# Kernel optimization log

Hardware: AMD Instinct MI355X
Metric: run time of the kernel (lower is better)

The kernel has to match this reference:

```python
import jax, jax.numpy as jnp
import numpy as np

DIM = 1024
T, B = 1024, 32


def setup_inputs() -> dict:
    key = jax.random.key(0)
    ks = jax.random.split(key, 6)
    x = jax.random.normal(ks[0], (T, B, DIM), dtype=jnp.float32)
    h0 = jnp.zeros((B, DIM), dtype=jnp.float32)
    W_zr = 0.02 * jax.random.normal(ks[1], (2 * DIM, DIM), dtype=jnp.float32)
    U_zr = 0.02 * jax.random.normal(ks[2], (2 * DIM, DIM), dtype=jnp.float32)
    W_h = 0.02 * jax.random.normal(ks[3], (DIM, DIM), dtype=jnp.float32)
    U_h = 0.02 * jax.random.normal(ks[4], (DIM, DIM), dtype=jnp.float32)
    b_zr = jnp.zeros((2 * DIM,), dtype=jnp.float32)
    b_h = jnp.zeros((DIM,), dtype=jnp.float32)
    return {"x": x, "h0": h0, "W_zr": W_zr, "U_zr": U_zr,
            "W_h": W_h, "U_h": U_h, "b_zr": b_zr, "b_h": b_h}


def _gru(x, h0, W_zr, U_zr, W_h, U_h, b_zr, b_h):
    dim = h0.shape[-1]
    # Precompute input projections for all timesteps (batched GEMM).
    xzr = jnp.einsum('tbd,ed->tbe', x, W_zr) + b_zr   # [T,B,2D]
    xh = jnp.einsum('tbd,ed->tbe', x, W_h) + b_h      # [T,B,D]
    U_z, U_r = U_zr[:dim], U_zr[dim:]

    def step(h_prev, inputs):
        xzr_t, xh_t = inputs
        z = jax.nn.sigmoid(xzr_t[:, :dim] + h_prev @ U_z.T)
        r = jax.nn.sigmoid(xzr_t[:, dim:] + h_prev @ U_r.T)
        h_tilde = jnp.tanh(xh_t + (r * h_prev) @ U_h.T)
        h = (1.0 - z) * h_prev + z * h_tilde
        return h, h

    _, hs = jax.lax.scan(step, h0, (xzr, xh))
    return hs  # [T,B,D]


def reference(x, h0, W_zr, U_zr, W_h, U_h, b_zr, b_h):
    return _gru(x, h0, W_zr, U_zr, W_h, U_h, b_zr, b_h)
```

## Files before the change

kernel.cpp:

```cpp
#include <hip/hip_runtime.h>


typedef __attribute__((ext_vector_type(8))) __bf16 bf16x8;
typedef __attribute__((ext_vector_type(4))) float f32x4;
typedef unsigned short ushort_t;
typedef unsigned long long u64;

#define DIM_ 1024
#define BATCH_ 32
#define T_ 1024
#define NC_ 3072

static constexpr size_t OFF_P     = 0;
static constexpr size_t OFF_XBF   = 201326592;
static constexpr size_t OFF_WBF   = OFF_XBF + 67108864;
static constexpr size_t OFF_UZR   = OFF_WBF + 6291456;
static constexpr size_t OFF_UH    = OFF_UZR + 4194304;
static constexpr size_t OFF_HB    = OFF_UH  + 2097152;
static constexpr size_t OFF_RH    = OFF_HB  + 65536;
static constexpr size_t OFF_FLAGS = OFF_RH  + 65536;

__device__ __forceinline__ float b2f(ushort_t u) {
  union { float f; unsigned i; } v;
  v.i = ((unsigned)u) << 16;
  return v.f;
}
__device__ __forceinline__ ushort_t f2b(float f) {
  union { float f; unsigned i; } v;
  v.f = f;
  unsigned r = v.i + 0x7fffu + ((v.i >> 16) & 1u);
  return (ushort_t)(r >> 16);
}

__device__ __forceinline__ void st_u32_sc(void* p, unsigned v) {
  asm volatile("global_store_dword %0, %1, off sc0 sc1" ::"v"(p), "v"(v)
               : "memory");
}
__device__ __forceinline__ unsigned ld_u32_sc(const void* p) {
  unsigned r;
  asm volatile("global_load_dword %0, %1, off sc0 sc1\n\ts_waitcnt vmcnt(0)"
               : "=v"(r) : "v"(p) : "memory");
  return r;
}
__device__ __forceinline__ u64 ld_u64_sc(const void* p) {
  u64 r;
  asm volatile("global_load_dwordx2 %0, %1, off sc0 sc1" : "=v"(r) : "v"(p));
  return r;
}
__device__ __forceinline__ void vm_drain() {
  asm volatile("s_waitcnt vmcnt(0)" ::: "memory");
}

__global__ void cvt_f32_bf16x4(const float4* __restrict__ src,
                               uint2* __restrict__ dst, int n4) {
  int i = blockIdx.x * blockDim.x + threadIdx.x;
  int st = gridDim.x * blockDim.x;
  for (; i < n4; i += st) {
    float4 v = src[i];
    unsigned a = (unsigned)f2b(v.x) | ((unsigned)f2b(v.y) << 16);
    unsigned b = (unsigned)f2b(v.z) | ((unsigned)f2b(v.w) << 16);
    dst[i] = make_uint2(a, b);
  }
}

__global__ void zero_flags(unsigned* f) { f[threadIdx.x] = 0u; }

__global__ __launch_bounds__(256) void gemm_xw(
    const ushort_t* __restrict__ A, const ushort_t* __restrict__ Bm,
    const float* __restrict__ bzr, const float* __restrict__ bh,
    ushort_t* __restrict__ C) {
  __shared__ ushort_t As[128][40];
  __shared__ ushort_t Bs[128][40];
  const int bi = blockIdx.x;
  const int p = bi / 192;
  const int q = bi % 192;
  const int i0 = (p * 8 + (q & 7)) * 128;
  const int n0 = (q >> 3) * 128;
  const int tid = threadIdx.x;
  const int w = tid >> 6, l = tid & 63;
  const int wr = w >> 1, wc = w & 1;
  const int quad = l >> 4, lr = l & 15;

  f32x4 acc[4][4] = {};
  for (int kc = 0; kc < 1024; kc += 32) {
    __syncthreads();
#pragma unroll
    for (int j = 0; j < 2; ++j) {
      int c = j * 256 + tid;
      int r = c >> 2, pp = c & 3;
      *(int4*)(&As[r][pp * 8]) =
          *(const int4*)(A + (size_t)(i0 + r) * 1024 + kc + pp * 8);
      *(int4*)(&Bs[r][pp * 8]) =
          *(const int4*)(Bm + (size_t)(n0 + r) * 1024 + kc + pp * 8);
    }
    __syncthreads();
    bf16x8 af[4], bfr[4];
#pragma unroll
    for (int mb = 0; mb < 4; ++mb)
      af[mb] = *(const bf16x8*)(&As[wr * 64 + mb * 16 + lr][quad * 8]);
#pragma unroll
    for (int nb = 0; nb < 4; ++nb)
      bfr[nb] = *(const bf16x8*)(&Bs[wc * 64 + nb * 16 + lr][quad * 8]);
#pragma unroll
    for (int mb = 0; mb < 4; ++mb)
#pragma unroll
      for (int nb = 0; nb < 4; ++nb)
        acc[mb][nb] = __builtin_amdgcn_mfma_f32_16x16x32_bf16(
            af[mb], bfr[nb], acc[mb][nb], 0, 0, 0);
  }
#pragma unroll
  for (int nb = 0; nb < 4; ++nb) {
    int col = n0 + wc * 64 + nb * 16 + lr;
    float bias = (col < 2048) ? bzr[col] : bh[col - 2048];
#pragma unroll
    for (int mb = 0; mb < 4; ++mb) {
#pragma unroll
      for (int reg = 0; reg < 4; ++reg) {
        int row = i0 + wr * 64 + mb * 16 + quad * 4 + reg;
        C[(size_t)row * NC_ + col] = f2b(acc[mb][nb][reg] + bias);
      }
    }
  }
}

__device__ __forceinline__ void group_barrier(unsigned* gflags, int gg,
                                              unsigned gen, int tid) {
  vm_drain();
  __syncthreads();
  if (tid == 0) st_u32_sc(gflags + gg, gen);
  if (tid < 32) {
    while (ld_u32_sc(gflags + tid) < gen) __builtin_amdgcn_s_sleep(1);
  }
  __syncthreads();
}

__global__ __launch_bounds__(256, 1) void gru_scan(
    const ushort_t* __restrict__ P, const ushort_t* __restrict__ Uzr,
    const ushort_t* __restrict__ Uh, const float* __restrict__ h0,
    ushort_t* __restrict__ Hb, ushort_t* __restrict__ RH,
    unsigned* __restrict__ flags, float* __restrict__ out) {
  const int g = blockIdx.x;
  const int G = g >> 5, gg = g & 31;
  const int rb0 = G * 16;
  const int cs = gg * 32;
  const int tid = threadIdx.x;
  const int w = tid >> 6, l = tid & 63;
  const int quad = l >> 4, lr = l & 15;
  unsigned* gflags = flags + G * 32;

  __shared__ ushort_t StageL[16][1032];
  __shared__ float Hl[16][33];
  __shared__ f32x4 red[2][64];

  const int ctA = w >> 1, cbA = w & 1;
  const int khB = w >> 1, cbB = w & 1;
  const int eA = cs + cbA * 16 + lr;
  const int eB = cs + cbB * 16 + lr;

  bf16x8 wa[32];
  {
    const ushort_t* urow = Uzr + (size_t)(ctA * 1024 + eA) * DIM_;
#pragma unroll
    for (int it = 0; it < 32; ++it)
      wa[it] = *(const bf16x8*)(urow + it * 32 + quad * 8);
  }
  bf16x8 wb[16];
  {
    const ushort_t* urow = Uh + (size_t)eB * DIM_ + khB * 512;
#pragma unroll
    for (int it = 0; it < 16; ++it)
      wb[it] = *(const bf16x8*)(urow + it * 32 + quad * 8);
  }

  {
    int rr = tid >> 4, cp = tid & 15;
    int c0 = cp * 2;
    float v0 = h0[(rb0 + rr) * DIM_ + cs + c0];
    float v1 = h0[(rb0 + rr) * DIM_ + cs + c0 + 1];
    Hl[rr][c0] = v0;
    Hl[rr][c0 + 1] = v1;
    unsigned pk = (unsigned)f2b(v0) | ((unsigned)f2b(v1) << 16);
    st_u32_sc(&Hb[(size_t)(rb0 + rr) * DIM_ + cs + c0], pk);
  }

  float pA[4], pB[4];
  {
    const size_t prow = (size_t)rb0 * NC_;
#pragma unroll
    for (int reg = 0; reg < 4; ++reg) {
      int br = quad * 4 + reg;
      pA[reg] = b2f(P[prow + (size_t)br * NC_ + ctA * 1024 + eA]);
      pB[reg] = b2f(P[prow + (size_t)br * NC_ + 2048 + eB]);
    }
  }

  unsigned gen = 1;
  group_barrier(gflags, gg, gen, tid);

  for (int t = 0; t < T_; ++t) {
    {
      u64 tmp[16];
#pragma unroll
      for (int j = 0; j < 16; ++j)
        tmp[j] =
            ld_u64_sc((const u64*)(Hb + (size_t)(rb0 + j) * DIM_) + tid);
      vm_drain();
#pragma unroll
      for (int j = 0; j < 16; ++j) *(u64*)&StageL[j][tid * 4] = tmp[j];
    }
    __syncthreads();

    f32x4 acc = {0.f, 0.f, 0.f, 0.f};
#pragma unroll
    for (int it = 0; it < 32; ++it) {
      bf16x8 a = *(const bf16x8*)&StageL[lr][it * 32 + quad * 8];
      acc = __builtin_amdgcn_mfma_f32_16x16x32_bf16(a, wa[it], acc, 0, 0, 0);
    }
    float zv[4];
#pragma unroll
    for (int reg = 0; reg < 4; ++reg) {
      int br = quad * 4 + reg;
      float pre = acc[reg] + pA[reg];
      float sv = 1.f / (1.f + __expf(-pre));
      if (ctA == 0) {
        zv[reg] = sv;
      } else {
        float hv = Hl[br][cbA * 16 + lr];
        unsigned own = f2b(sv * hv);
        unsigned oth = (unsigned)__shfl_xor((int)own, 1);
        if ((l & 1) == 0) {
          unsigned pk = own | (oth << 16);
          st_u32_sc(&RH[(size_t)(rb0 + br) * DIM_ + eA], pk);
        }
      }
    }
    ++gen;
    group_barrier(gflags, gg, gen, tid);

    {
      u64 tmp[16];
#pragma unroll
      for (int j = 0; j < 16; ++j)
        tmp[j] =
            ld_u64_sc((const u64*)(RH + (size_t)(rb0 + j) * DIM_) + tid);
      vm_drain();
#pragma unroll
      for (int j = 0; j < 16; ++j) *(u64*)&StageL[j][tid * 4] = tmp[j];
    }
    __syncthreads();

    f32x4 acch = {0.f, 0.f, 0.f, 0.f};
#pragma unroll
    for (int it = 0; it < 16; ++it) {
      bf16x8 a = *(const bf16x8*)&StageL[lr][khB * 512 + it * 32 + quad * 8];
      acch = __builtin_amdgcn_mfma_f32_16x16x32_bf16(a, wb[it], acch, 0, 0, 0);
    }
    if (w >= 2) red[cbB][l] = acch;
    __syncthreads();
    if (w < 2) {
      f32x4 oth4 = red[cbB][l];
#pragma unroll
      for (int reg = 0; reg < 4; ++reg) {
        int br = quad * 4 + reg;
        float ax = pB[reg] + acch[reg] + oth4[reg];
        float e = __expf(2.f * fabsf(ax));
        float th = copysignf(1.f - 2.f / (e + 1.f), ax);
        float hv = Hl[br][cbB * 16 + lr];
        float z = zv[reg];
        float hn = (1.f - z) * hv + z * th;
        Hl[br][cbB * 16 + lr] = hn;
        int gb = rb0 + br;
        unsigned own = f2b(hn);
        unsigned otherh = (unsigned)__shfl_xor((int)own, 1);
        float hn_oth = __shfl_xor(hn, 1);
        if ((l & 1) == 0) {
          st_u32_sc(&Hb[(size_t)gb * DIM_ + eB], own | (otherh << 16));
          *(float2*)&out[((size_t)t * BATCH_ + gb) * DIM_ + eB] =
              make_float2(hn, hn_oth);
        }
      }
    }

    {
      int tn = (t + 1 < T_) ? t + 1 : t;
      const size_t prow = ((size_t)(tn * BATCH_ + rb0)) * NC_;
#pragma unroll
      for (int reg = 0; reg < 4; ++reg) {
        int br = quad * 4 + reg;
        pA[reg] = b2f(P[prow + (size_t)br * NC_ + ctA * 1024 + eA]);
        pB[reg] = b2f(P[prow + (size_t)br * NC_ + 2048 + eB]);
      }
    }
    ++gen;
    group_barrier(gflags, gg, gen, tid);
  }
}

extern "C" void kernel_launch(void* const* d_in, const int* in_sizes, int n_in,
                              void* d_out, int out_size, void* d_ws,
                              size_t ws_size, hipStream_t stream) {
  const float* x   = (const float*)d_in[0];
  const float* h0  = (const float*)d_in[1];
  const float* Wzr = (const float*)d_in[2];
  const float* Uzr = (const float*)d_in[3];
  const float* Wh  = (const float*)d_in[4];
  const float* Uh  = (const float*)d_in[5];
  const float* bzr = (const float*)d_in[6];
  const float* bh  = (const float*)d_in[7];
  char* ws = (char*)d_ws;
  ushort_t* P     = (ushort_t*)(ws + OFF_P);
  ushort_t* Xbf   = (ushort_t*)(ws + OFF_XBF);
  ushort_t* Wbf   = (ushort_t*)(ws + OFF_WBF);
  ushort_t* Uzrb  = (ushort_t*)(ws + OFF_UZR);
  ushort_t* Uhb   = (ushort_t*)(ws + OFF_UH);
  ushort_t* Hb    = (ushort_t*)(ws + OFF_HB);
  ushort_t* RH    = (ushort_t*)(ws + OFF_RH);
  unsigned* flags = (unsigned*)(ws + OFF_FLAGS);
  float* out = (float*)d_out;

  zero_flags<<<1, 64, 0, stream>>>(flags);
  cvt_f32_bf16x4<<<1024, 256, 0, stream>>>((const float4*)x, (uint2*)Xbf,
                                           33554432 / 4);
  cvt_f32_bf16x4<<<256, 256, 0, stream>>>((const float4*)Wzr, (uint2*)Wbf,
                                          2097152 / 4);
  cvt_f32_bf16x4<<<128, 256, 0, stream>>>((const float4*)Wh,
                                          (uint2*)(Wbf + 2097152), 1048576 / 4);
  cvt_f32_bf16x4<<<256, 256, 0, stream>>>((const float4*)Uzr, (uint2*)Uzrb,
                                          2097152 / 4);
  cvt_f32_bf16x4<<<128, 256, 0, stream>>>((const float4*)Uh, (uint2*)Uhb,
                                          1048576 / 4);
  gemm_xw<<<6144, 256, 0, stream>>>(Xbf, Wbf, bzr, bh, P);
  gru_scan<<<64, 256, 0, stream>>>(P, Uzrb, Uhb, h0, Hb, RH, flags, out);
}
```

Measured before the change: 7.691 ms.

## Replace flag barriers with per-element tagged data in recurrent GRU scan

```diff
diff --git a/kernel.cpp b/kernel.cpp
--- a/kernel.cpp
+++ b/kernel.cpp
@@ -3,8 +3,8 @@
 
 typedef __attribute__((ext_vector_type(8))) __bf16 bf16x8;
 typedef __attribute__((ext_vector_type(4))) float f32x4;
+typedef __attribute__((ext_vector_type(4))) unsigned u32x4;
 typedef unsigned short ushort_t;
-typedef unsigned long long u64;
 
 #define DIM_ 1024
 #define BATCH_ 32
@@ -16,9 +16,8 @@
 static constexpr size_t OFF_WBF   = OFF_XBF + 67108864;
 static constexpr size_t OFF_UZR   = OFF_WBF + 6291456;
 static constexpr size_t OFF_UH    = OFF_UZR + 4194304;
-static constexpr size_t OFF_HB    = OFF_UH  + 2097152;
-static constexpr size_t OFF_RH    = OFF_HB  + 65536;
-static constexpr size_t OFF_FLAGS = OFF_RH  + 65536;
+static constexpr size_t OFF_HBT   = OFF_UH  + 2097152;
+static constexpr size_t OFF_RHT   = OFF_HBT + 131072;
 
 __device__ __forceinline__ float b2f(ushort_t u) {
   union { float f; unsigned i; } v;
@@ -36,19 +35,18 @@
   asm volatile("global_store_dword %0, %1, off sc0 sc1" ::"v"(p), "v"(v)
                : "memory");
 }
-__device__ __forceinline__ unsigned ld_u32_sc(const void* p) {
-  unsigned r;
-  asm volatile("global_load_dword %0, %1, off sc0 sc1\n\ts_waitcnt vmcnt(0)"
+__device__ __forceinline__ u32x4 ld_u128_sc(const void* p) {
+  u32x4 r;
+  asm volatile("global_load_dwordx4 %0, %1, off sc0 sc1"
                : "=v"(r) : "v"(p) : "memory");
   return r;
 }
-__device__ __forceinline__ u64 ld_u64_sc(const void* p) {
-  u64 r;
-  asm volatile("global_load_dwordx2 %0, %1, off sc0 sc1" : "=v"(r) : "v"(p));
-  return r;
-}
 __device__ __forceinline__ void vm_drain() {
   asm volatile("s_waitcnt vmcnt(0)" ::: "memory");
+}
+__device__ __forceinline__ bool tags_ok(u32x4 a, unsigned g) {
+  unsigned m = (a.x ^ g) | (a.y ^ g) | (a.z ^ g) | (a.w ^ g);
+  return (m & 0xFFFFu) == 0u;
 }
 
 __global__ void cvt_f32_bf16x4(const float4* __restrict__ src,
@@ -62,8 +60,6 @@
     dst[i] = make_uint2(a, b);
   }
 }
-
-__global__ void zero_flags(unsigned* f) { f[threadIdx.x] = 0u; }
 
 __global__ __launch_bounds__(256) void gemm_xw(
     const ushort_t* __restrict__ A, const ushort_t* __restrict__ Bm,
@@ -123,22 +119,11 @@
   }
 }
 
-__device__ __forceinline__ void group_barrier(unsigned* gflags, int gg,
-                                              unsigned gen, int tid) {
-  vm_drain();
-  __syncthreads();
-  if (tid == 0) st_u32_sc(gflags + gg, gen);
-  if (tid < 32) {
-    while (ld_u32_sc(gflags + tid) < gen) __builtin_amdgcn_s_sleep(1);
-  }
-  __syncthreads();
-}
-
 __global__ __launch_bounds__(256, 1) void gru_scan(
     const ushort_t* __restrict__ P, const ushort_t* __restrict__ Uzr,
     const ushort_t* __restrict__ Uh, const float* __restrict__ h0,
-    ushort_t* __restrict__ Hb, ushort_t* __restrict__ RH,
-    unsigned* __restrict__ flags, float* __restrict__ out) {
+    unsigned* __restrict__ HbT, unsigned* __restrict__ RHT,
+    float* __restrict__ out) {
   const int g = blockIdx.x;
   const int G = g >> 5, gg = g & 31;
   const int rb0 = G * 16;
@@ -146,7 +131,8 @@
   const int tid = threadIdx.x;
   const int w = tid >> 6, l = tid & 63;
   const int quad = l >> 4, lr = l & 15;
-  unsigned* gflags = flags + G * 32;
+  unsigned* HbT_g = HbT + G * 16384;
+  unsigned* RHT_g = RHT + G * 16384;
 
   __shared__ ushort_t StageL[16][1032];
   __shared__ float Hl[16][33];
@@ -156,6 +142,7 @@
   const int khB = w >> 1, cbB = w & 1;
   const int eA = cs + cbA * 16 + lr;
   const int eB = cs + cbB * 16 + lr;
+  const int c0 = tid * 4;
 
   bf16x8 wa[32];
   {
@@ -173,14 +160,14 @@
   }
 
   {
-    int rr = tid >> 4, cp = tid & 15;
-    int c0 = cp * 2;
-    float v0 = h0[(rb0 + rr) * DIM_ + cs + c0];
-    float v1 = h0[(rb0 + rr) * DIM_ + cs + c0 + 1];
-    Hl[rr][c0] = v0;
-    Hl[rr][c0 + 1] = v1;
-    unsigned pk = (unsigned)f2b(v0) | ((unsigned)f2b(v1) << 16);
-    st_u32_sc(&Hb[(size_t)(rb0 + rr) * DIM_ + cs + c0], pk);
+    int s0 = tid * 2;
+    int rr = s0 >> 5, cc = s0 & 31;
+    float v0 = h0[(rb0 + rr) * DIM_ + cs + cc];
+    float v1 = h0[(rb0 + rr) * DIM_ + cs + cc + 1];
+    Hl[rr][cc] = v0;
+    Hl[rr][cc + 1] = v1;
+    st_u32_sc(&HbT_g[rr * 1024 + cs + cc], ((unsigned)f2b(v0) << 16));
+    st_u32_sc(&HbT_g[rr * 1024 + cs + cc + 1], ((unsigned)f2b(v1) << 16));
   }
 
   float pA[4], pB[4];
@@ -194,28 +181,46 @@
     }
   }
 
-  unsigned gen = 1;
-  group_barrier(gflags, gg, gen, tid);
-
   for (int t = 0; t < T_; ++t) {
+    const unsigned tagH = (unsigned)(t & 0xFFFF);
+    const unsigned tagR = (unsigned)(t & 0xFFFF);
+    const unsigned tagH1 = (unsigned)((t + 1) & 0xFFFF);
+
+    __syncthreads();
     {
-      u64 tmp[16];
-#pragma unroll
-      for (int j = 0; j < 16; ++j)
-        tmp[j] =
-            ld_u64_sc((const u64*)(Hb + (size_t)(rb0 + j) * DIM_) + tid);
+      const unsigned* src = HbT_g + c0;
+      u32x4 tmp[16];
+#pragma unroll
+      for (int j = 0; j < 16; ++j) tmp[j] = ld_u128_sc(src + j * 1024);
       vm_drain();
 #pragma unroll
-      for (int j = 0; j < 16; ++j) *(u64*)&StageL[j][tid * 4] = tmp[j];
-    }
-    __syncthreads();
-
-    f32x4 acc = {0.f, 0.f, 0.f, 0.f};
-#pragma unroll
-    for (int it = 0; it < 32; ++it) {
-      bf16x8 a = *(const bf16x8*)&StageL[lr][it * 32 + quad * 8];
-      acc = __builtin_amdgcn_mfma_f32_16x16x32_bf16(a, wa[it], acc, 0, 0, 0);
-    }
+      for (int j = 0; j < 16; ++j) {
+        u32x4 v = tmp[j];
+        while (!tags_ok(v, tagH)) {
+          v = ld_u128_sc(src + j * 1024);
+          vm_drain();
+        }
+        tmp[j] = v;
+      }
+#pragma unroll
+      for (int j = 0; j < 16; ++j) {
+        unsigned lo = (tmp[j].x >> 16) | (tmp[j].y & 0xFFFF0000u);
+        unsigned hi = (tmp[j].z >> 16) | (tmp[j].w & 0xFFFF0000u);
+        *(uint2*)&StageL[j][c0] = make_uint2(lo, hi);
+      }
+    }
+    __syncthreads();
+
+    f32x4 acc0 = {0.f, 0.f, 0.f, 0.f}, acc1 = {0.f, 0.f, 0.f, 0.f};
+#pragma unroll
+    for (int it = 0; it < 32; it += 2) {
+      bf16x8 a0 = *(const bf16x8*)&StageL[lr][it * 32 + quad * 8];
+      bf16x8 a1 = *(const bf16x8*)&StageL[lr][(it + 1) * 32 + quad * 8];
+      acc0 = __builtin_amdgcn_mfma_f32_16x16x32_bf16(a0, wa[it], acc0, 0, 0, 0);
+      acc1 =
+          __builtin_amdgcn_mfma_f32_16x16x32_bf16(a1, wa[it + 1], acc1, 0, 0, 0);
+    }
+    f32x4 acc = acc0 + acc1;
     float zv[4];
 #pragma unroll
     for (int reg = 0; reg < 4; ++reg) {
@@ -226,35 +231,46 @@
         zv[reg] = sv;
       } else {
         float hv = Hl[br][cbA * 16 + lr];
-        unsigned own = f2b(sv * hv);
-        unsigned oth = (unsigned)__shfl_xor((int)own, 1);
-        if ((l & 1) == 0) {
-          unsigned pk = own | (oth << 16);
-          st_u32_sc(&RH[(size_t)(rb0 + br) * DIM_ + eA], pk);
+        st_u32_sc(&RHT_g[br * 1024 + eA],
+                  ((unsigned)f2b(sv * hv) << 16) | tagR);
+      }
+    }
+
+    __syncthreads();
+    {
+      const unsigned* src = RHT_g + c0;
+      u32x4 tmp[16];
+#pragma unroll
+      for (int j = 0; j < 16; ++j) tmp[j] = ld_u128_sc(src + j * 1024);
+      vm_drain();
+#pragma unroll
+      for (int j = 0; j < 16; ++j) {
+        u32x4 v = tmp[j];
+        while (!tags_ok(v, tagR)) {
+          v = ld_u128_sc(src + j * 1024);
+          vm_drain();
         }
-      }
-    }
-    ++gen;
-    group_barrier(gflags, gg, gen, tid);
-
-    {
-      u64 tmp[16];
-#pragma unroll
-      for (int j = 0; j < 16; ++j)
-        tmp[j] =
-            ld_u64_sc((const u64*)(RH + (size_t)(rb0 + j) * DIM_) + tid);
-      vm_drain();
-#pragma unroll
-      for (int j = 0; j < 16; ++j) *(u64*)&StageL[j][tid * 4] = tmp[j];
-    }
-    __syncthreads();
-
-    f32x4 acch = {0.f, 0.f, 0.f, 0.f};
-#pragma unroll
-    for (int it = 0; it < 16; ++it) {
-      bf16x8 a = *(const bf16x8*)&StageL[lr][khB * 512 + it * 32 + quad * 8];
-      acch = __builtin_amdgcn_mfma_f32_16x16x32_bf16(a, wb[it], acch, 0, 0, 0);
-    }
+        tmp[j] = v;
+      }
+#pragma unroll
+      for (int j = 0; j < 16; ++j) {
+        unsigned lo = (tmp[j].x >> 16) | (tmp[j].y & 0xFFFF0000u);
+        unsigned hi = (tmp[j].z >> 16) | (tmp[j].w & 0xFFFF0000u);
+        *(uint2*)&StageL[j][c0] = make_uint2(lo, hi);
+      }
+    }
+    __syncthreads();
+
+    f32x4 b0 = {0.f, 0.f, 0.f, 0.f}, b1 = {0.f, 0.f, 0.f, 0.f};
+#pragma unroll
+    for (int it = 0; it < 16; it += 2) {
+      bf16x8 a0 = *(const bf16x8*)&StageL[lr][khB * 512 + it * 32 + quad * 8];
+      bf16x8 a1 =
+          *(const bf16x8*)&StageL[lr][khB * 512 + (it + 1) * 32 + quad * 8];
+      b0 = __builtin_amdgcn_mfma_f32_16x16x32_bf16(a0, wb[it], b0, 0, 0, 0);
+      b1 = __builtin_amdgcn_mfma_f32_16x16x32_bf16(a1, wb[it + 1], b1, 0, 0, 0);
+    }
+    f32x4 acch = b0 + b1;
     if (w >= 2) red[cbB][l] = acch;
     __syncthreads();
     if (w < 2) {
@@ -269,15 +285,8 @@
         float z = zv[reg];
         float hn = (1.f - z) * hv + z * th;
         Hl[br][cbB * 16 + lr] = hn;
-        int gb = rb0 + br;
-        unsigned own = f2b(hn);
-        unsigned otherh = (unsigned)__shfl_xor((int)own, 1);
-        float hn_oth = __shfl_xor(hn, 1);
-        if ((l & 1) == 0) {
-          st_u32_sc(&Hb[(size_t)gb * DIM_ + eB], own | (otherh << 16));
-          *(float2*)&out[((size_t)t * BATCH_ + gb) * DIM_ + eB] =
-              make_float2(hn, hn_oth);
-        }
+        st_u32_sc(&HbT_g[br * 1024 + eB], ((unsigned)f2b(hn) << 16) | tagH1);
+        out[((size_t)t * BATCH_ + rb0 + br) * DIM_ + eB] = hn;
       }
     }
 
@@ -291,8 +300,6 @@
         pB[reg] = b2f(P[prow + (size_t)br * NC_ + 2048 + eB]);
       }
     }
-    ++gen;
-    group_barrier(gflags, gg, gen, tid);
   }
 }
 
@@ -313,12 +320,10 @@
   ushort_t* Wbf   = (ushort_t*)(ws + OFF_WBF);
   ushort_t* Uzrb  = (ushort_t*)(ws + OFF_UZR);
   ushort_t* Uhb   = (ushort_t*)(ws + OFF_UH);
-  ushort_t* Hb    = (ushort_t*)(ws + OFF_HB);
-  ushort_t* RH    = (ushort_t*)(ws + OFF_RH);
-  unsigned* flags = (unsigned*)(ws + OFF_FLAGS);
+  unsigned* HbT   = (unsigned*)(ws + OFF_HBT);
+  unsigned* RHT   = (unsigned*)(ws + OFF_RHT);
   float* out = (float*)d_out;
 
-  zero_flags<<<1, 64, 0, stream>>>(flags);
   cvt_f32_bf16x4<<<1024, 256, 0, stream>>>((const float4*)x, (uint2*)Xbf,
                                            33554432 / 4);
   cvt_f32_bf16x4<<<256, 256, 0, stream>>>((const float4*)Wzr, (uint2*)Wbf,
@@ -330,5 +335,5 @@
   cvt_f32_bf16x4<<<128, 256, 0, stream>>>((const float4*)Uh, (uint2*)Uhb,
                                           1048576 / 4);
   gemm_xw<<<6144, 256, 0, stream>>>(Xbf, Wbf, bzr, bh, P);
-  gru_scan<<<64, 256, 0, stream>>>(P, Uzrb, Uhb, h0, Hb, RH, flags, out);
-}
+  gru_scan<<<64, 256, 0, stream>>>(P, Uzrb, Uhb, h0, HbT, RHT, out);
+}
```

After: 12.84 ms. 67.0% more time.
